# Performance work log

Hardware: AMD Instinct MI355X
Metric: run time of the kernel (lower is better)

## Reference

```python
import jax, jax.numpy as jnp
import numpy as np

C = 256
CQK = C // 8  # query/key channels from Conv2d(in_dim, in_dim//8, 1)


def _cross_attn(x, y, qw, qb, kw, kb, vw, vb, gamma):
    # x, y: [B, C, H, W]; 1x1 convs are channel matmuls
    B, Cc, H, W = x.shape
    N = H * W
    xf = x.reshape(B, Cc, N)
    yf = y.reshape(B, Cc, N)
    q = jnp.einsum('oc,bcn->bno', qw, xf) + qb  # [B, N, CQK]
    k = jnp.einsum('oc,bcn->bon', kw, yf) + kb[:, None]  # [B, CQK, N]
    energy = jnp.einsum('bnc,bcm->bnm', q, k)  # [B, N, N]
    attn = jax.nn.softmax(energy, axis=2)
    v = jnp.einsum('oc,bcn->bon', vw, yf) + vb[:, None]  # [B, C, N]
    out = jnp.einsum('bcm,bnm->bcn', v, attn)  # value @ attention^T
    out = out.reshape(B, Cc, H, W)
    return gamma * out + x


def setup_inputs() -> dict:
    key = jax.random.key(0)
    ks = jax.random.split(key, 16)
    B, H, W = 4, 64, 64
    s = 1.0 / np.sqrt(C)
    d = {
        'x': jax.random.normal(ks[0], (B, C, H, W), jnp.float32),
        'y': jax.random.normal(ks[1], (B, C, H, W), jnp.float32),
        'z': jax.random.normal(ks[2], (B, C, H, W), jnp.float32),
        'q1_w': jax.random.normal(ks[3], (CQK, C), jnp.float32) * s,
        'q1_b': jax.random.normal(ks[4], (CQK,), jnp.float32) * s,
        'k1_w': jax.random.normal(ks[5], (CQK, C), jnp.float32) * s,
        'k1_b': jax.random.normal(ks[6], (CQK,), jnp.float32) * s,
        'v1_w': jax.random.normal(ks[7], (C, C), jnp.float32) * s,
        'v1_b': jax.random.normal(ks[8], (C,), jnp.float32) * s,
        'gamma1': jax.random.normal(ks[9], (1,), jnp.float32) * 0.1,
        'q2_w': jax.random.normal(ks[10], (CQK, C), jnp.float32) * s,
        'q2_b': jax.random.normal(ks[11], (CQK,), jnp.float32) * s,
        'k2_w': jax.random.normal(ks[12], (CQK, C), jnp.float32) * s,
        'k2_b': jax.random.normal(ks[13], (CQK,), jnp.float32) * s,
        'v2_w': jax.random.normal(ks[14], (C, C), jnp.float32) * s,
        'v2_b': jax.random.normal(ks[15], (C,), jnp.float32) * s,
        'gamma2': jax.random.normal(jax.random.fold_in(key, 99), (1,), jnp.float32) * 0.1,
    }
    return d


def reference(x, y, z, q1_w, q1_b, k1_w, k1_b, v1_w, v1_b, gamma1,
              q2_w, q2_b, k2_w, k2_b, v2_w, v2_b, gamma2):
    out1 = _cross_attn(x, y, q1_w, q1_b, k1_w, k1_b, v1_w, v1_b, gamma1)
    out2 = _cross_attn(out1, z, q2_w, q2_b, k2_w, k2_b, v2_w, v2_b, gamma2)
    return out2
```

## Files before the change

### kernel.cpp

```cpp
#include <hip/hip_runtime.h>
#include <hip/hip_bf16.h>

#define NSEQ 4096
#define CDIM 256
#define CQKD 32
#define LOG2E 1.4426950408889634f

typedef float v4f __attribute__((ext_vector_type(4)));
typedef float v16f __attribute__((ext_vector_type(16)));
typedef short v8s __attribute__((ext_vector_type(8)));
typedef unsigned long long u64;

__device__ __forceinline__ float exp2_(float x) {
#if __has_builtin(__builtin_amdgcn_exp2f)
  return __builtin_amdgcn_exp2f(x);
#else
  float r;
  __asm__("v_exp_f32 %0, %1" : "=v"(r) : "v"(x));
  return r;
#endif
}

__device__ __forceinline__ unsigned short f2bf(float x) {
  unsigned u = __builtin_bit_cast(unsigned, x);
  unsigned r = (u + 0x7FFFu + ((u >> 16) & 1u)) >> 16;
  return (unsigned short)r;
}
__device__ __forceinline__ float bf2f(unsigned short s) {
  unsigned u = ((unsigned)s) << 16;
  return __builtin_bit_cast(float, u);
}
__device__ __forceinline__ unsigned int pack_bf16(float a, float b) {
#if __has_builtin(__builtin_amdgcn_cvt_pk_bf16_f32)
  typedef __bf16 v2bf __attribute__((ext_vector_type(2)));
  v2bf r = __builtin_amdgcn_cvt_pk_bf16_f32(a, b);
  return __builtin_bit_cast(unsigned int, r);
#else
  return ((unsigned)f2bf(b) << 16) | (unsigned)f2bf(a);
#endif
}

__device__ __forceinline__ unsigned char f2e4m3(float x) {
  unsigned u = __builtin_bit_cast(unsigned, x);
  unsigned s = (u >> 24) & 0x80u;
  unsigned au = u & 0x7fffffffu;
  if (au > 0x43e00000u) return (unsigned char)(s | 0x7eu);
  if (au < 0x3c800000u) {
    float ax = __builtin_bit_cast(float, au);
    int q = (int)(ax * 512.0f + 0.5f);
    if (q > 7) q = 7;
    return (unsigned char)(s | (unsigned)q);
  }
  int e = (int)((au >> 23) & 0xffu) - 127 + 7;
  unsigned m = au & 0x7fffffu;
  unsigned mr = m + 0x7ffffu + ((m >> 20) & 1u);
  if (mr >= 0x800000u) { mr -= 0x800000u; e += 1; if (e >= 16) return (unsigned char)(s | 0x7e); }
  return (unsigned char)(s | ((unsigned)e << 3) | (mr >> 20));
}
__device__ __forceinline__ unsigned int pack4_fp8(float a, float b, float c, float d) {
#if __has_builtin(__builtin_amdgcn_cvt_pk_fp8_f32)
  int v = 0;
  v = __builtin_amdgcn_cvt_pk_fp8_f32(a, b, v, false);
  v = __builtin_amdgcn_cvt_pk_fp8_f32(c, d, v, true);
  return (unsigned int)v;
#else
  return (unsigned)f2e4m3(a) | ((unsigned)f2e4m3(b) << 8) |
         ((unsigned)f2e4m3(c) << 16) | ((unsigned)f2e4m3(d) << 24);
#endif
}

__global__ __launch_bounds__(256) void convw_kernel(
    const float* __restrict__ q1w, const float* __restrict__ k1w,
    const float* __restrict__ k2w, const float* __restrict__ q2w,
    const float* __restrict__ v1w, const float* __restrict__ v2w,
    unsigned short* __restrict__ W) {
  const int s = blockIdx.x * 256 + threadIdx.x;
  const float* src;
  int o, ch0;
  size_t obase;
  float scale = 1.0f;
  if (s < 3072) {
    const int wsel = s >> 10, r = s & 1023;
    src = wsel == 0 ? q1w : (wsel == 1 ? k1w : k2w);
    const int ot = r >> 9, cb = (r >> 6) & 7, lane = r & 63;
    o = ot * 16 + (lane & 15);
    ch0 = cb * 32 + ((lane >> 4) & 3) * 8;
    obase = (size_t)wsel * 8192 + (size_t)r * 8;
  } else if (s < 19456) {
    const int s2 = s - 3072, which = s2 >> 13, r = s2 & 8191;
    src = which == 0 ? v1w : v2w;
    const int ot = r >> 9, cb = (r >> 6) & 7, lane = r & 63;
    o = ot * 16 + (lane & 15);
    ch0 = cb * 32 + ((lane >> 4) & 3) * 8;
    obase = 32768 + (size_t)which * 65536 + (size_t)r * 8;
  } else {
    const int r = s - 19456;
    src = q2w;
    const int lane = r & 63;
    o = lane & 31;
    ch0 = (r >> 6) * 16 + (lane >> 5) * 8;
    obase = 24576 + (size_t)r * 8;
    scale = LOG2E;
  }
#pragma unroll
  for (int j = 0; j < 8; ++j)
    W[obase + j] = f2bf(src[o * CDIM + ch0 + j] * scale);
}

__global__ __launch_bounds__(256) void prep_kernel(
    const float* __restrict__ x, const float* __restrict__ y,
    const float* __restrict__ z, const unsigned short* __restrict__ Wbf,
    const float* __restrict__ q1b, const float* __restrict__ k1b,
    const float* __restrict__ k2b, const float* __restrict__ v1b,
    const float* __restrict__ v2b, unsigned short* __restrict__ Q1,
    unsigned short* __restrict__ K1, unsigned short* __restrict__ K2,
    unsigned char* __restrict__ V1, unsigned char* __restrict__ V2) {
  __shared__ unsigned short t[256][72];
  __shared__ unsigned short Kt[64][40];
  const int src = blockIdx.z;
  const float* in = src == 0 ? x : (src == 1 ? y : z);
  const int b = blockIdx.y;
  const int n0 = blockIdx.x * 64;
  const int tid = threadIdx.x, lane = tid & 63, w = tid >> 6;
  const int quad = lane >> 4, r15 = lane & 15, l31 = lane & 31, lh = lane >> 5;
  const float* ip = in + (size_t)(b * CDIM) * NSEQ + n0;
  {
    const int chb = tid >> 4, c4 = (tid & 15) * 4;
#pragma unroll
    for (int p = 0; p < 16; ++p) {
      const int ch = p * 16 + chb;
      float4 v = *(const float4*)(ip + (size_t)ch * NSEQ + c4);
      uint2 pk;
      pk.x = pack_bf16(v.x, v.y);
      pk.y = pack_bf16(v.z, v.w);
      *(uint2*)&t[ch][c4] = pk;
    }
  }
  __syncthreads();
  v8s af[8];
#pragma unroll
  for (int cb = 0; cb < 8; ++cb) {
    union { unsigned short e[8]; v8s v; } u;
#pragma unroll
    for (int j = 0; j < 8; ++j) u.e[j] = t[cb * 32 + quad * 8 + j][w * 16 + r15];
    af[cb] = u.v;
  }
  const int nt = blockIdx.x * 4 + w;
  const unsigned short* Wqk = Wbf + src * 8192;
  v4f a0 = {0.f, 0.f, 0.f, 0.f}, a1 = a0;
#pragma unroll
  for (int cb = 0; cb < 8; ++cb) {
    v8s b0 = *(const v8s*)(Wqk + (size_t)cb * 512 + lane * 8);
    v8s b1 = *(const v8s*)(Wqk + (size_t)(8 + cb) * 512 + lane * 8);
    a0 = __builtin_amdgcn_mfma_f32_16x16x32_bf16(af[cb], b0, a0, 0, 0, 0);
    a1 = __builtin_amdgcn_mfma_f32_16x16x32_bf16(af[cb], b1, a1, 0, 0, 0);
  }
  if (src == 0) {
#pragma unroll
    for (int r = 0; r < 4; ++r) {
      Q1[((size_t)b * NSEQ + nt * 16 + quad * 4 + r) * CQKD + r15] =
          f2bf((a0[r] + q1b[r15]) * LOG2E);
      Q1[((size_t)b * NSEQ + nt * 16 + quad * 4 + r) * CQKD + 16 + r15] =
          f2bf((a1[r] + q1b[16 + r15]) * LOG2E);
    }
    return;
  }
  const float* kbias = src == 1 ? k1b : k2b;
#pragma unroll
  for (int r = 0; r < 4; ++r) {
    Kt[w * 16 + quad * 4 + r][r15] = f2bf(a0[r] + kbias[r15]);
    Kt[w * 16 + quad * 4 + r][16 + r15] = f2bf(a1[r] + kbias[16 + r15]);
  }
  const unsigned short* Wv = Wbf + 32768 + (src - 1) * 65536;
  const float* vbias = src == 1 ? v1b : v2b;
  v4f vacc[16];
#pragma unroll
  for (int ot = 0; ot < 16; ++ot) vacc[ot] = (v4f){0.f, 0.f, 0.f, 0.f};
#pragma unroll
  for (int cb = 0; cb < 8; ++cb) {
    const v8s afc = af[cb];
#pragma unroll
    for (int ot = 0; ot < 16; ++ot) {
      v8s bf = *(const v8s*)(Wv + (size_t)(ot * 8 + cb) * 512 + lane * 8);
      vacc[ot] = __builtin_amdgcn_mfma_f32_16x16x32_bf16(afc, bf, vacc[ot], 0, 0, 0);
    }
  }
  __syncthreads();
  unsigned char* Vt8 = (unsigned char*)t;
#pragma unroll
  for (int ot = 0; ot < 16; ++ot) {
    const int ch = ot * 16 + r15;
    const float bv = vbias[ch];
    *(unsigned int*)&Vt8[(size_t)ch * 72 + w * 16 + quad * 4] =
        pack4_fp8(vacc[ot][0] + bv, vacc[ot][1] + bv, vacc[ot][2] + bv, vacc[ot][3] + bv);
  }
  {
    unsigned short* Kout = (src == 1 ? K1 : K2) + (size_t)b * (NSEQ / 16) * 512;
    *(v8s*)(Kout + ((size_t)nt * 64 + lane) * 8) = *(const v8s*)&Kt[w * 16 + r15][quad * 8];
  }
  __syncthreads();
  unsigned char* Vout = (src == 1 ? V1 : V2) + (size_t)b * (NSEQ / 16) * 8 * 512;
#pragma unroll
  for (int chb = 0; chb < 8; ++chb)
    *(u64*)(Vout + (((size_t)nt * 8 + chb) * 64 + lane) * 8) =
        *(const u64*)&Vt8[(size_t)(chb * 32 + l31) * 72 + w * 16 + lh * 8];
}


__device__ __forceinline__ void poll_ge(const unsigned* p, unsigned target) {
  for (int i = 0; i < (1 << 20); ++i) {
    unsigned v = __hip_atomic_load(p, __ATOMIC_RELAXED, __HIP_MEMORY_SCOPE_WORKGROUP);
    if (v >= target) break;
    __builtin_amdgcn_s_sleep(1);
  }
  __builtin_amdgcn_sched_barrier(0);
  __asm__ __volatile__("" ::: "memory");
}
__device__ __forceinline__ void signal_cnt(unsigned* p, int lane) {
  __asm__ __volatile__("s_waitcnt lgkmcnt(0)" ::: "memory");
  __builtin_amdgcn_sched_barrier(0);
  if (lane == 0)
    __hip_atomic_fetch_add(p, 1u, __ATOMIC_RELAXED, __HIP_MEMORY_SCOPE_WORKGROUP);
}

__device__ __forceinline__ void max_pass16(
    const unsigned short* __restrict__ Kp, const v8s qf[4], int w, int lane,
    float (*lbuf)[64], float m[4]) {
  const v4f vzero4 = {0.f, 0.f, 0.f, 0.f};
  const int r15 = lane & 15;
  const unsigned short* Kl = Kp + (size_t)w * 512 + lane * 8;
  v8s kA = *(const v8s*)(Kl);
  v8s kB = *(const v8s*)(Kl + 8192);
#pragma unroll
  for (int qt = 0; qt < 4; ++qt) m[qt] = -3.0e38f;
#pragma unroll 2
  for (int kt = 0; kt < 16; ++kt) {
    v8s kC = *(const v8s*)(Kl + (size_t)((kt + 2) & 15) * 8192);
#pragma unroll
    for (int qt = 0; qt < 4; ++qt) {
      v4f st = __builtin_amdgcn_mfma_f32_16x16x32_bf16(kA, qf[qt], vzero4, 0, 0, 0);
      m[qt] = fmaxf(m[qt], fmaxf(fmaxf(st[0], st[1]), fmaxf(st[2], st[3])));
    }
    kA = kB;
    kB = kC;
  }
#pragma unroll
  for (int qt = 0; qt < 4; ++qt) {
    m[qt] = fmaxf(m[qt], __shfl_xor(m[qt], 16));
    m[qt] = fmaxf(m[qt], __shfl_xor(m[qt], 32));
  }
  if (lane < 16) {
#pragma unroll
    for (int qt = 0; qt < 4; ++qt) lbuf[w][qt * 16 + lane] = m[qt];
  }
  __syncthreads();
#pragma unroll
  for (int qt = 0; qt < 4; ++qt) {
    float mm = lbuf[0][qt * 16 + r15];
#pragma unroll
    for (int ww = 1; ww < 16; ++ww) mm = fmaxf(mm, lbuf[ww][qt * 16 + r15]);
    m[qt] = mm;
  }
  __syncthreads();
}

__device__ __forceinline__ void s_phase(
    unsigned char* __restrict__ P, int pbuf, const v8s kf, const v8s qf[4],
    const float m[4], int w, int lane, float lsum[4]) {
  const v4f vzero4 = {0.f, 0.f, 0.f, 0.f};
  const int quad = lane >> 4, r15 = lane & 15;
  unsigned char* pw = P + pbuf * 8704 + w * 16 + quad * 4;
#pragma unroll
  for (int qt = 0; qt < 4; ++qt) {
    v4f st = __builtin_amdgcn_mfma_f32_16x16x32_bf16(kf, qf[qt], vzero4, 0, 0, 0);
    float e0 = exp2_(st[0] - m[qt]), e1 = exp2_(st[1] - m[qt]);
    float e2 = exp2_(st[2] - m[qt]), e3 = exp2_(st[3] - m[qt]);
    lsum[qt] += (e0 + e1) + (e2 + e3);
    *(unsigned int*)(pw + (size_t)(qt * 16 + r15) * 136) = pack4_fp8(e0, e1, e2, e3);
  }
}

__device__ __forceinline__ void pv_tile(
    const unsigned char* __restrict__ P, int pbuf, const u64 vf[8], int lane,
    v16f acc[2]) {
  const int l31 = lane & 31, lh = lane >> 5;
  const unsigned char* pb = P + pbuf * 8704;
  __builtin_amdgcn_s_setprio(1);
#pragma unroll
  for (int s = 0; s < 8; ++s) {
    long pf0 = (long)*(const u64*)(pb + (size_t)l31 * 136 + s * 16 + lh * 8);
    long pf1 = (long)*(const u64*)(pb + (size_t)(32 + l31) * 136 + s * 16 + lh * 8);
    acc[0] = __builtin_amdgcn_mfma_f32_32x32x16_fp8_fp8((long)vf[s], pf0, acc[0], 0, 0, 0);
    acc[1] = __builtin_amdgcn_mfma_f32_32x32x16_fp8_fp8((long)vf[s], pf1, acc[1], 0, 0, 0);
  }
  __builtin_amdgcn_s_setprio(0);
}

__device__ __forceinline__ void attn_loop(
    const unsigned short* __restrict__ Kp, const unsigned char* __restrict__ Vp,
    unsigned char* __restrict__ P, unsigned* __restrict__ prod_cnt,
    unsigned* __restrict__ cons_cnt, const v8s qf[4], const float m[4], int w,
    int lane, v16f acc[2], float lsum[4]) {
  if (w < 8) {
    const unsigned short* Kl = Kp + (size_t)w * 512 + lane * 8;
    v8s k0 = *(const v8s*)(Kl);
    v8s k1 = *(const v8s*)(Kl + 4096);
#pragma unroll 1
    for (int p = 0; p < 16; ++p) {
      const int slot = p & 3;
      const unsigned it = (unsigned)(p >> 2);
      v8s kn0 = *(const v8s*)(Kl + (size_t)((2 * p + 2) & 31) * 4096);
      v8s kn1 = *(const v8s*)(Kl + (size_t)((2 * p + 3) & 31) * 4096);
      poll_ge(&cons_cnt[slot], 8u * it);
      s_phase(P, 2 * slot, k0, qf, m, w, lane, lsum);
      s_phase(P, 2 * slot + 1, k1, qf, m, w, lane, lsum);
      signal_cnt(&prod_cnt[slot], lane);
      k0 = kn0;
      k1 = kn1;
    }
  } else {
    const unsigned char* Vl = Vp + (size_t)(w - 8) * 512 + lane * 8;
    u64 v0[8], v1[8];
#pragma unroll
    for (int s = 0; s < 8; ++s) v0[s] = *(const u64*)(Vl + (size_t)s * 4096);
#pragma unroll
    for (int s = 0; s < 8; ++s) v1[s] = *(const u64*)(Vl + 32768 + (size_t)s * 4096);
#pragma unroll 1
    for (int p = 0; p < 16; ++p) {
      const int slot = p & 3;
      const unsigned it = (unsigned)(p >> 2);
      poll_ge(&prod_cnt[slot], 8u * (it + 1));
      pv_tile(P, 2 * slot, v0, lane, acc);
#pragma unroll
      for (int s = 0; s < 8; ++s)
        v0[s] = *(const u64*)(Vl + (size_t)((2 * p + 2) & 31) * 32768 + s * 4096);
      pv_tile(P, 2 * slot + 1, v1, lane, acc);
#pragma unroll
      for (int s = 0; s < 8; ++s)
        v1[s] = *(const u64*)(Vl + (size_t)((2 * p + 3) & 31) * 32768 + s * 4096);
      signal_cnt(&cons_cnt[slot], lane);
    }
  }
}

__global__ __launch_bounds__(1024, 4) void fused_attn_kernel(
    const unsigned short* __restrict__ Q1g, const unsigned short* __restrict__ K1g,
    const unsigned char* __restrict__ V1g, const unsigned short* __restrict__ K2g,
    const unsigned char* __restrict__ V2g, const unsigned short* __restrict__ W2g,
    const float* __restrict__ x, const float* __restrict__ q2b,
    const float* __restrict__ g1p, const float* __restrict__ g2p,
    float* __restrict__ outp) {
  __shared__ __align__(16) unsigned char P[8 * 8704];
  __shared__ __align__(16) unsigned short out1T[64 * 264];
  __shared__ __align__(16) unsigned short q2s[64 * 32];
  __shared__ float lbuf[16][64];
  __shared__ unsigned prod_cnt[4], cons_cnt[4];

  const int tid = threadIdx.x;
  const int lane = tid & 63;
  const int w = tid >> 6;
  const int quad = lane >> 4;
  const int r15 = lane & 15;
  const int l31 = lane & 31, lh = lane >> 5;
  const int b = blockIdx.x & 3;
  const int n0 = (blockIdx.x >> 2) * 64;

  const float g1 = g1p[0];
  const float g2 = g2p[0];

  const unsigned short* Qp  = Q1g + (size_t)b * NSEQ * CQKD;
  const unsigned short* K1p = K1g + (size_t)b * (NSEQ / 16) * 512;
  const unsigned short* K2p = K2g + (size_t)b * (NSEQ / 16) * 512;
  const unsigned char* V1p  = V1g + (size_t)b * (NSEQ / 16) * 8 * 512;
  const unsigned char* V2p  = V2g + (size_t)b * (NSEQ / 16) * 8 * 512;

  v8s qf[4];
#pragma unroll
  for (int qt = 0; qt < 4; ++qt)
    qf[qt] = *(const v8s*)(Qp + (n0 + qt * 16 + r15) * CQKD + quad * 8);

  v16f acc[2];
  float lsum[4] = {0.f, 0.f, 0.f, 0.f};
  float m[4];
  acc[0] = (v16f)(0.f); acc[1] = (v16f)(0.f);

  if (tid < 4) { prod_cnt[tid] = 0; cons_cnt[tid] = 0; }
  max_pass16(K1p, qf, w, lane, lbuf, m);
  attn_loop(K1p, V1p, P, prod_cnt, cons_cnt, qf, m, w, lane, acc, lsum);
  if (w < 8) {
#pragma unroll
    for (int qt = 0; qt < 4; ++qt) {
      lsum[qt] += __shfl_xor(lsum[qt], 16);
      lsum[qt] += __shfl_xor(lsum[qt], 32);
    }
    if (lane < 16) {
#pragma unroll
      for (int qt = 0; qt < 4; ++qt) lbuf[w][qt * 16 + lane] = lsum[qt];
    }
  }
  __syncthreads();
  float rinv[2];
#pragma unroll
  for (int qh = 0; qh < 2; ++qh) {
    const int q = qh * 32 + l31;
    float d = 0.f;
#pragma unroll
    for (int ww = 0; ww < 8; ++ww) d += lbuf[ww][q];
    rinv[qh] = 1.0f / d;
  }
  if (w >= 8) {
    const int cw = (w - 8) * 32;
#pragma unroll
    for (int qh = 0; qh < 2; ++qh) {
      const int q = qh * 32 + l31;
#pragma unroll
      for (int rg = 0; rg < 4; ++rg) {
        const int c = cw + 8 * rg + 4 * lh;
        float o0 = g1 * (acc[qh][rg * 4 + 0] * rinv[qh]) + x[((size_t)b * CDIM + c + 0) * NSEQ + n0 + q];
        float o1 = g1 * (acc[qh][rg * 4 + 1] * rinv[qh]) + x[((size_t)b * CDIM + c + 1) * NSEQ + n0 + q];
        float o2 = g1 * (acc[qh][rg * 4 + 2] * rinv[qh]) + x[((size_t)b * CDIM + c + 2) * NSEQ + n0 + q];
        float o3 = g1 * (acc[qh][rg * 4 + 3] * rinv[qh]) + x[((size_t)b * CDIM + c + 3) * NSEQ + n0 + q];
        uint2 pk;
        pk.x = pack_bf16(o0, o1);
        pk.y = pack_bf16(o2, o3);
        *(uint2*)(out1T + (size_t)q * 264 + c) = pk;
      }
    }
  }
  __syncthreads();

  if (w < 2) {
    const int qh = w;
    v16f qacc = (v16f)(0.f);
#pragma unroll
    for (int s = 0; s < 16; ++s) {
      v8s af = *(const v8s*)(W2g + (size_t)(s * 64 + lane) * 8);
      v8s bf = *(const v8s*)(out1T + (size_t)(qh * 32 + l31) * 264 + s * 16 + lh * 8);
      qacc = __builtin_amdgcn_mfma_f32_32x32x16_bf16(af, bf, qacc, 0, 0, 0);
    }
#pragma unroll
    for (int rg = 0; rg < 4; ++rg) {
      const int o = 8 * rg + 4 * lh;
      uint2 pk;
      pk.x = pack_bf16(qacc[rg * 4 + 0] + q2b[o + 0] * LOG2E, qacc[rg * 4 + 1] + q2b[o + 1] * LOG2E);
      pk.y = pack_bf16(qacc[rg * 4 + 2] + q2b[o + 2] * LOG2E, qacc[rg * 4 + 3] + q2b[o + 3] * LOG2E);
      *(uint2*)(q2s + (size_t)(qh * 32 + l31) * 32 + o) = pk;
    }
  }
  __syncthreads();

#pragma unroll
  for (int qt = 0; qt < 4; ++qt)
    qf[qt] = *(const v8s*)(q2s + (qt * 16 + r15) * 32 + quad * 8);
  acc[0] = (v16f)(0.f); acc[1] = (v16f)(0.f);
#pragma unroll
  for (int qt = 0; qt < 4; ++qt) lsum[qt] = 0.f;
  if (tid < 4) { prod_cnt[tid] = 0; cons_cnt[tid] = 0; }
  max_pass16(K2p, qf, w, lane, lbuf, m);
  attn_loop(K2p, V2p, P, prod_cnt, cons_cnt, qf, m, w, lane, acc, lsum);
  if (w < 8) {
#pragma unroll
    for (int qt = 0; qt < 4; ++qt) {
      lsum[qt] += __shfl_xor(lsum[qt], 16);
      lsum[qt] += __shfl_xor(lsum[qt], 32);
    }
    if (lane < 16) {
#pragma unroll
      for (int qt = 0; qt < 4; ++qt) lbuf[w][qt * 16 + lane] = lsum[qt];
    }
  }
  __syncthreads();
#pragma unroll
  for (int qh = 0; qh < 2; ++qh) {
    const int q = qh * 32 + l31;
    float d = 0.f;
#pragma unroll
    for (int ww = 0; ww < 8; ++ww) d += lbuf[ww][q];
    rinv[qh] = 1.0f / d;
  }
  if (w >= 8) {
    const int cw = (w - 8) * 32;
#pragma unroll
    for (int qh = 0; qh < 2; ++qh) {
      const int q = qh * 32 + l31;
#pragma unroll
      for (int rg = 0; rg < 4; ++rg) {
        const int c = cw + 8 * rg + 4 * lh;
#pragma unroll
        for (int i = 0; i < 4; ++i) {
          float res = bf2f(out1T[(size_t)q * 264 + c + i]);
          outp[((size_t)b * CDIM + c + i) * NSEQ + n0 + q] =
              g2 * (acc[qh][rg * 4 + i] * rinv[qh]) + res;
        }
      }
    }
  }
}

extern "C" void kernel_launch(void* const* d_in, const int* in_sizes, int n_in,
                              void* d_out, int out_size, void* d_ws, size_t ws_size,
                              hipStream_t stream) {
  const float* x   = (const float*)d_in[0];
  const float* y   = (const float*)d_in[1];
  const float* z   = (const float*)d_in[2];
  const float* q1w = (const float*)d_in[3];
  const float* q1b = (const float*)d_in[4];
  const float* k1w = (const float*)d_in[5];
  const float* k1b = (const float*)d_in[6];
  const float* v1w = (const float*)d_in[7];
  const float* v1b = (const float*)d_in[8];
  const float* g1  = (const float*)d_in[9];
  const float* q2w = (const float*)d_in[10];
  const float* q2b = (const float*)d_in[11];
  const float* k2w = (const float*)d_in[12];
  const float* k2b = (const float*)d_in[13];
  const float* v2w = (const float*)d_in[14];
  const float* v2b = (const float*)d_in[15];
  const float* g2  = (const float*)d_in[16];
  char* ws = (char*)d_ws;
  unsigned short* Wbf = (unsigned short*)(ws);
  unsigned short* Q1  = (unsigned short*)(ws + 327680);
  unsigned short* K1  = (unsigned short*)(ws + 1376256);
  unsigned short* K2  = (unsigned short*)(ws + 2424832);
  unsigned char*  V1  = (unsigned char*)(ws + 3473408);
  unsigned char*  V2  = (unsigned char*)(ws + 7667712);
  float* outp = (float*)d_out;

  convw_kernel<<<dim3(80), 256, 0, stream>>>(q1w, k1w, k2w, q2w, v1w, v2w, Wbf);
  prep_kernel<<<dim3(64, 4, 3), 256, 0, stream>>>(x, y, z, Wbf, q1b, k1b, k2b, v1b,
                                                  v2b, Q1, K1, K2, V1, V2);
  fused_attn_kernel<<<dim3(256), 1024, 0, stream>>>(Q1, K1, V1, K2, V2, Wbf + 24576, x,
                                                    q2b, g1, g2, outp);
}
```

Before: 207.2 us.

## Use scaled 32x32x64 fp8 MFMA for PV and relayout V accordingly

Replaces the sixteen 32x32x16 fp8 MFMAs per PV tile with four mfma_scale 32x32x64 f8f6f4 instructions using unit scales (0x7f). The V projection output is rewritten in a new global layout so each lane loads 32 contiguous bytes, and P is read as 32-byte chunks per lane. The aim is to double MFMA throughput for the PV product and cut instruction count, at the cost of wider register operands and a changed layout contract between kernels.

```diff
diff --git a/kernel.cpp b/kernel.cpp
--- a/kernel.cpp
+++ b/kernel.cpp
@@ -9,6 +9,7 @@
 typedef float v4f __attribute__((ext_vector_type(4)));
 typedef float v16f __attribute__((ext_vector_type(16)));
 typedef short v8s __attribute__((ext_vector_type(8)));
+typedef int v8i __attribute__((ext_vector_type(8)));
 typedef unsigned long long u64;
 
 __device__ __forceinline__ float exp2_(float x) {
@@ -199,11 +200,19 @@
     *(v8s*)(Kout + ((size_t)nt * 64 + lane) * 8) = *(const v8s*)&Kt[w * 16 + r15][quad * 8];
   }
   __syncthreads();
-  unsigned char* Vout = (src == 1 ? V1 : V2) + (size_t)b * (NSEQ / 16) * 8 * 512;
-#pragma unroll
-  for (int chb = 0; chb < 8; ++chb)
-    *(u64*)(Vout + (((size_t)nt * 8 + chb) * 64 + lane) * 8) =
-        *(const u64*)&Vt8[(size_t)(chb * 32 + l31) * 72 + w * 16 + lh * 8];
+  unsigned char* Vout = (src == 1 ? V1 : V2) + (size_t)b * (NSEQ / 16) * 8 * 512 +
+                        (size_t)blockIdx.x * 16384;
+#pragma unroll
+  for (int h = 0; h < 2; ++h) {
+    const int chb = w * 2 + h;
+    u64 tmp[4];
+#pragma unroll
+    for (int j = 0; j < 4; ++j)
+      tmp[j] = *(const u64*)&Vt8[(size_t)(chb * 32 + l31) * 72 + lh * 32 + j * 8];
+#pragma unroll
+    for (int j = 0; j < 4; ++j)
+      *(u64*)(Vout + ((size_t)chb * 64 + lane) * 32 + j * 8) = tmp[j];
+  }
 }
 
 
@@ -281,18 +290,27 @@
 }
 
 __device__ __forceinline__ void pv_tile(
-    const unsigned char* __restrict__ P, int pbuf, const u64 vf[8], int lane,
+    const unsigned char* __restrict__ P, int pbuf, v8i a0, v8i a1, int lane,
     v16f acc[2]) {
   const int l31 = lane & 31, lh = lane >> 5;
   const unsigned char* pb = P + pbuf * 8704;
+  union { u64 d[4]; v8i v; } b00, b01, b10, b11;
+#pragma unroll
+  for (int j = 0; j < 4; ++j) {
+    b00.d[j] = *(const u64*)(pb + (size_t)l31 * 136 + lh * 32 + j * 8);
+    b01.d[j] = *(const u64*)(pb + (size_t)l31 * 136 + 64 + lh * 32 + j * 8);
+    b10.d[j] = *(const u64*)(pb + (size_t)(32 + l31) * 136 + lh * 32 + j * 8);
+    b11.d[j] = *(const u64*)(pb + (size_t)(32 + l31) * 136 + 64 + lh * 32 + j * 8);
+  }
   __builtin_amdgcn_s_setprio(1);
-#pragma unroll
-  for (int s = 0; s < 8; ++s) {
-    long pf0 = (long)*(const u64*)(pb + (size_t)l31 * 136 + s * 16 + lh * 8);
-    long pf1 = (long)*(const u64*)(pb + (size_t)(32 + l31) * 136 + s * 16 + lh * 8);
-    acc[0] = __builtin_amdgcn_mfma_f32_32x32x16_fp8_fp8((long)vf[s], pf0, acc[0], 0, 0, 0);
-    acc[1] = __builtin_amdgcn_mfma_f32_32x32x16_fp8_fp8((long)vf[s], pf1, acc[1], 0, 0, 0);
-  }
+  acc[0] = __builtin_amdgcn_mfma_scale_f32_32x32x64_f8f6f4(
+      a0, b00.v, acc[0], 0, 0, 0, 0x7f7f7f7f, 0, 0x7f7f7f7f);
+  acc[0] = __builtin_amdgcn_mfma_scale_f32_32x32x64_f8f6f4(
+      a1, b01.v, acc[0], 0, 0, 0, 0x7f7f7f7f, 0, 0x7f7f7f7f);
+  acc[1] = __builtin_amdgcn_mfma_scale_f32_32x32x64_f8f6f4(
+      a0, b10.v, acc[1], 0, 0, 0, 0x7f7f7f7f, 0, 0x7f7f7f7f);
+  acc[1] = __builtin_amdgcn_mfma_scale_f32_32x32x64_f8f6f4(
+      a1, b11.v, acc[1], 0, 0, 0, 0x7f7f7f7f, 0, 0x7f7f7f7f);
   __builtin_amdgcn_s_setprio(0);
 }
 
@@ -319,25 +337,22 @@
       k1 = kn1;
     }
   } else {
-    const unsigned char* Vl = Vp + (size_t)(w - 8) * 512 + lane * 8;
-    u64 v0[8], v1[8];
-#pragma unroll
-    for (int s = 0; s < 8; ++s) v0[s] = *(const u64*)(Vl + (size_t)s * 4096);
-#pragma unroll
-    for (int s = 0; s < 8; ++s) v1[s] = *(const u64*)(Vl + 32768 + (size_t)s * 4096);
+    const unsigned char* Vl = Vp + (size_t)(w - 8) * 2048 + (size_t)lane * 32;
+    v8i a00 = *(const v8i*)(Vl);
+    v8i a01 = *(const v8i*)(Vl + 16384);
+    v8i a10 = *(const v8i*)(Vl + 2 * 16384);
+    v8i a11 = *(const v8i*)(Vl + 3 * 16384);
 #pragma unroll 1
     for (int p = 0; p < 16; ++p) {
       const int slot = p & 3;
       const unsigned it = (unsigned)(p >> 2);
       poll_ge(&prod_cnt[slot], 8u * (it + 1));
-      pv_tile(P, 2 * slot, v0, lane, acc);
-#pragma unroll
-      for (int s = 0; s < 8; ++s)
-        v0[s] = *(const u64*)(Vl + (size_t)((2 * p + 2) & 31) * 32768 + s * 4096);
-      pv_tile(P, 2 * slot + 1, v1, lane, acc);
-#pragma unroll
-      for (int s = 0; s < 8; ++s)
-        v1[s] = *(const u64*)(Vl + (size_t)((2 * p + 3) & 31) * 32768 + s * 4096);
+      pv_tile(P, 2 * slot, a00, a01, lane, acc);
+      a00 = *(const v8i*)(Vl + (size_t)((4 * p + 4) & 63) * 16384);
+      a01 = *(const v8i*)(Vl + (size_t)((4 * p + 5) & 63) * 16384);
+      pv_tile(P, 2 * slot + 1, a10, a11, lane, acc);
+      a10 = *(const v8i*)(Vl + (size_t)((4 * p + 6) & 63) * 16384);
+      a11 = *(const v8i*)(Vl + (size_t)((4 * p + 7) & 63) * 16384);
       signal_cnt(&cons_cnt[slot], lane);
     }
   }
```

New measurement: 381.4 us. +84.0%, slower.
